# Optimization experiments

Hardware: AMD Instinct MI355X
Metric: run time of the kernel (lower is better)

## Reference

```python
import jax, jax.numpy as jnp
import numpy as np
from jax import lax

B = 256
NUM_CLASSES = 10
IN_CAPS = 32 * 6 * 6  # 1152
IN_DIM = 8
OUT_DIM = 16
NUM_ITERS = 3


def squash(t, axis=-1):
    sq = jnp.sum(t * t, axis=axis, keepdims=True)
    return (sq / (1.0 + sq)) * t / jnp.sqrt(sq)


def conv2d(x, w, b, stride):
    y = lax.conv_general_dilated(x, w, (stride, stride), 'VALID',
                                 dimension_numbers=('NCHW', 'OIHW', 'NCHW'))
    return y + b[None, :, None, None]


def setup_inputs() -> dict:
    key = jax.random.key(0)
    ks = jax.random.split(key, 12)
    f = jnp.float32
    return {
        'x': jax.random.uniform(ks[0], (B, 1, 28, 28), dtype=f),
        'conv1_w': jax.random.normal(ks[1], (256, 1, 9, 9), dtype=f) * 0.05,
        'conv1_b': jnp.zeros((256,), dtype=f),
        'prim_w': jax.random.normal(ks[2], (IN_DIM * 32, 256, 9, 9), dtype=f) * 0.02,
        'prim_b': jnp.zeros((IN_DIM * 32,), dtype=f),
        'route_w': jax.random.normal(ks[3], (NUM_CLASSES, IN_CAPS, IN_DIM, OUT_DIM), dtype=f),
        'dec_w1': jax.random.normal(ks[4], (OUT_DIM * NUM_CLASSES, 512), dtype=f) * 0.05,
        'dec_b1': jnp.zeros((512,), dtype=f),
        'dec_w2': jax.random.normal(ks[5], (512, 1024), dtype=f) * 0.04,
        'dec_b2': jnp.zeros((1024,), dtype=f),
        'dec_w3': jax.random.normal(ks[6], (1024, 28 * 28), dtype=f) * 0.03,
        'dec_b3': jnp.zeros((28 * 28,), dtype=f),
    }


def reference(x, conv1_w, conv1_b, prim_w, prim_b, route_w,
              dec_w1, dec_b1, dec_w2, dec_b2, dec_w3, dec_b3):
    bsz = x.shape[0]
    # conv1 + relu -> [B,256,20,20]
    h = jax.nn.relu(conv2d(x, conv1_w, conv1_b, 1))
    # primary capsules: 8 parallel convs (stacked into one) -> [B, 8*32, 6, 6]
    p = conv2d(h, prim_w, prim_b, 2)
    # each capsule conv flattens to [B, 32*36], concatenated along last dim
    p = p.reshape(bsz, IN_DIM, 32 * 6 * 6).transpose(0, 2, 1)  # [B, 1152, 8]
    u = squash(p, axis=-1)
    # priors: [o, b, i, d_out]
    priors = jnp.einsum('bic,oicd->obid', u, route_w)
    # routing by agreement: softmax over in_capsules (dim i), per original code
    logits = jnp.zeros((NUM_CLASSES, bsz, IN_CAPS, 1), dtype=priors.dtype)
    outputs = None
    for it in range(NUM_ITERS):
        probs = jax.nn.softmax(logits, axis=2)              # [o,b,i,1]
        outputs = squash(jnp.sum(probs * priors, axis=2, keepdims=True))  # [o,b,1,d]
        if it != NUM_ITERS - 1:
            logits = logits + jnp.sum(priors * outputs, axis=-1, keepdims=True)
    vecs = outputs.reshape(NUM_CLASSES, bsz, OUT_DIM).transpose(1, 0, 2)  # [B,10,16]
    classes = jnp.sqrt(jnp.sum(vecs * vecs, axis=-1))
    classes = jax.nn.softmax(classes, axis=1)               # [B,10]
    # y=None path: one-hot of predicted class (non-differentiable mask)
    y = jax.nn.one_hot(jnp.argmax(classes, axis=1), NUM_CLASSES, dtype=vecs.dtype)
    dec_in = (vecs * y[:, :, None]).reshape(bsz, -1)        # [B,160]
    hdec = jax.nn.relu(dec_in @ dec_w1 + dec_b1)
    hdec = jax.nn.relu(hdec @ dec_w2 + dec_b2)
    reconstruction = jax.nn.sigmoid(hdec @ dec_w3 + dec_b3)  # [B,784]
    return classes, reconstruction
```

## Files before the change

### kernel.cpp

```cpp
#include <hip/hip_runtime.h>
#include <hip/hip_bf16.h>
#include <math.h>


typedef __attribute__((ext_vector_type(8))) short bf16x8;
typedef __attribute__((ext_vector_type(4))) float f32x4;

__device__ __forceinline__ void gl16(const void* g, void* l) {
  __builtin_amdgcn_global_load_lds((const __attribute__((address_space(1))) void*)g,
                                   (__attribute__((address_space(3))) void*)l,
                                   16, 0, 0);
}

__global__ __launch_bounds__(256) void k_conv1(const float* __restrict__ x,
                                               const float* __restrict__ w,
                                               const float* __restrict__ bias,
                                               __hip_bfloat16* __restrict__ hT) {
  const int bid = blockIdx.x;
  const int img = bid >> 2, ocq = bid & 3;
  __shared__ float xs[784];
  __shared__ float ws[64 * 81];
  const int t = threadIdx.x;
  const float4* xg = (const float4*)(x + (size_t)img * 784);
  if (t < 196) ((float4*)xs)[t] = xg[t];
  const float4* wg = (const float4*)(w + (size_t)ocq * 64 * 81);
  for (int i = t; i < 1296; i += 256) ((float4*)ws)[i] = wg[i];
  __syncthreads();
  const int ocl = t & 63, rowg = t >> 6;
  const int oc = ocq * 64 + ocl;
  const int ch = oc >> 3, icl = oc & 7;
  const float bv = bias[oc];
  __hip_bfloat16* hb = hT + ((size_t)img * 32 + ch) * 6560 + icl;
#pragma unroll 1
  for (int r = rowg; r < 20; r += 4) {
    float acc[20];
#pragma unroll
    for (int p = 0; p < 20; p++) acc[p] = bv;
#pragma unroll
    for (int ky = 0; ky < 9; ky++) {
      float xr[28];
      const float* xrow = &xs[(r + ky) * 28];
#pragma unroll
      for (int q = 0; q < 7; q++) ((float4*)xr)[q] = ((const float4*)xrow)[q];
      float wr[9];
#pragma unroll
      for (int i = 0; i < 9; i++) wr[i] = ws[ocl * 81 + ky * 9 + i];
#pragma unroll
      for (int kx = 0; kx < 9; kx++)
#pragma unroll
        for (int p = 0; p < 20; p++)
          acc[p] = fmaf(wr[kx], xr[p + kx], acc[p]);
    }
#pragma unroll
    for (int p = 0; p < 20; p++) {
      const float v = fmaxf(acc[p], 0.f);
      const __hip_bfloat16 hi = __float2bfloat16(v);
      const __hip_bfloat16 lo = __float2bfloat16(v - __bfloat162float(hi));
      __hip_bfloat16* dst = hb + (size_t)(p * 41 + r * 2) * 8;
      dst[0] = hi;
      dst[8] = lo;
    }
  }
}

__global__ __launch_bounds__(256) void k_wrep(const float* __restrict__ pw,
                                              __hip_bfloat16* __restrict__ wGp) {
  const int s = blockIdx.x >> 2, ocq = blockIdx.x & 3;
  const int ch = s / 21, tq = s - ch * 21;
  __hip_bfloat16* outp = wGp + ((size_t)s * 4 + ocq) * 4608;
  const int t = threadIdx.x;
  for (int e = t; e < 2048; e += 256) {
    const int ocl = e >> 5, k = e & 31;
    const int tapl = k >> 3, icl = k & 7;
    const int tap = tq * 4 + tapl, ic = ch * 8 + icl;
    const int oc = ocq * 64 + ocl;
    const float v = (tap < 81) ? pw[((size_t)oc * 256 + ic) * 81 + tap] : 0.f;
    const __hip_bfloat16 hi = __float2bfloat16(v);
    const __hip_bfloat16 lo = __float2bfloat16(v - __bfloat162float(hi));
    outp[ocl * 72 + k] = hi;
    outp[ocl * 72 + 32 + k] = lo;
  }
  for (int e = t; e < 512; e += 256) {
    const int ocl = e >> 3, j = e & 7;
    outp[ocl * 72 + 64 + j] = __float2bfloat16(0.f);
  }
}

#define HT_B 52480
#define PQ_F 2359296
__global__ __launch_bounds__(512) void k_conv2(
    const __hip_bfloat16* __restrict__ hTg,
    const __hip_bfloat16* __restrict__ wGp,
    float* __restrict__ pq, int c0) {
  __shared__ char hT[HT_B];
  const int bid = blockIdx.x;
  int ig, ocq, kq;
  if (gridDim.x == 512) {
    ig = (bid & 7) | (((bid >> 5) & 7) << 3);
    ocq = (bid >> 3) & 3;
    kq = bid >> 8;
  } else {
    ig = bid >> 3;
    ocq = (bid >> 1) & 3;
    kq = bid & 1;
  }
  const int t = threadIdx.x;
  const int w = t >> 6, lane = t & 63;
  const int lquad = lane >> 4, lrow = lane & 15;
  const int mhalf = w >> 2;
  const int nt = mhalf ? 4 : 5;
  const int mtb = mhalf ? 5 : 0;
  const int ocg = ocq * 64 + (w & 3) * 16 + lrow;
  int abase[5];
#pragma unroll
  for (int i = 0; i < 5; i++) {
    int m = (mtb + i) * 16 + lrow;
    if (i >= nt) m = 0;
    const int img = m / 36, px = m - img * 36;
    const int oy = px / 6, ox = px - oy * 6;
    abase[i] = img * 13120 + ox * 1312 + oy * 64;
  }
  f32x4 acc[5];
#pragma unroll
  for (int i = 0; i < 5; i++) acc[i] = (f32x4){0.f, 0.f, 0.f, 0.f};

  const char* hgc = (const char*)hTg;
  const char* wp = (const char*)wGp + ((size_t)(kq * 336) * 4 + ocq) * 4608 +
                   ((w & 3) * 16 + lrow) * 144 + lquad * 16;
  bf16x8 bh = *(const bf16x8*)wp;
  bf16x8 bl = *(const bf16x8*)(wp + 64);
  wp += 18432;
#pragma unroll 1
  for (int chl = 0; chl < 16; chl++) {
    const int ch = kq * 16 + chl;
    const char* hch = hgc + ((size_t)(ig * 128) + ch) * 13120;
#pragma unroll
    for (int rr = 0; rr < 6; rr++) {
      const int idx = t + rr * 512;
      const int j = idx / 820, r = idx - j * 820;
      gl16(hch + (size_t)j * 419840 + r * 16, hT + rr * 8192 + w * 1024);
    }
    if (t < 208) {
      const int idx = 3072 + t;
      const int j = idx / 820, r = idx - j * 820;
      gl16(hch + (size_t)j * 419840 + r * 16, hT + 49152 + w * 1024);
    }
    __syncthreads();
#pragma unroll 1
    for (int tq = 0; tq < 21; tq++) {
      const bf16x8 nh = *(const bf16x8*)wp;
      const bf16x8 nl = *(const bf16x8*)(wp + 64);
      wp += 18432;
      const int tt = tq * 4 + lquad;
      const int ky = tt / 9, kx = tt - ky * 9;
      const int toff = kx * 656 + ky * 32;
      bf16x8 ah[5];
#pragma unroll
      for (int i = 0; i < 5; i++)
        ah[i] = *(const bf16x8*)(hT + abase[i] + toff);
#pragma unroll
      for (int i = 0; i < 5; i++)
        if (i < nt) acc[i] = __builtin_amdgcn_mfma_f32_16x16x32_bf16(ah[i], bh, acc[i], 0, 0, 0);
#pragma unroll
      for (int i = 0; i < 5; i++)
        if (i < nt) acc[i] = __builtin_amdgcn_mfma_f32_16x16x32_bf16(ah[i], bl, acc[i], 0, 0, 0);
      bf16x8 al[5];
#pragma unroll
      for (int i = 0; i < 5; i++)
        al[i] = *(const bf16x8*)(hT + abase[i] + toff + 16);
#pragma unroll
      for (int i = 0; i < 5; i++)
        if (i < nt) acc[i] = __builtin_amdgcn_mfma_f32_16x16x32_bf16(al[i], bh, acc[i], 0, 0, 0);
      bh = nh;
      bl = nl;
    }
    __syncthreads();
  }
  float* pblk = pq + (size_t)kq * PQ_F;
#pragma unroll
  for (int i = 0; i < 5; i++) {
    if (i < nt) {
#pragma unroll
      for (int r = 0; r < 4; r++) {
        const int m = (mtb + i) * 16 + lquad * 4 + r;
        const int img = m / 36, px = m - img * 36;
        pblk[((size_t)(c0 + ig * 4 + img) * 36 + px) * 256 + ocg] = acc[i][r];
      }
    }
  }
}

__global__ __launch_bounds__(256) void k_squash(const float* __restrict__ pq,
                                                const float* __restrict__ bias,
                                                float* __restrict__ u) {
  const int gid = blockIdx.x * 256 + threadIdx.x;
  const int b = gid / 1152, i = gid - b * 1152;
  const int cp = i / 36, px = i - cp * 36;
  const float* pb = pq + ((size_t)b * 36 + px) * 256 + cp;
  float s[8];
#pragma unroll
  for (int d = 0; d < 8; d++)
    s[d] = pb[d * 32] + pb[(size_t)PQ_F + d * 32] + bias[cp + d * 32];
  float sq = 0.f;
#pragma unroll
  for (int d = 0; d < 8; d++) sq = fmaf(s[d], s[d], sq);
  const float scale = sq / ((1.f + sq) * sqrtf(sq));
  float o[8];
#pragma unroll
  for (int d = 0; d < 8; d++) o[d] = s[d] * scale;
  float* ub = u + (size_t)gid * 8;
  ((float4*)ub)[0] = ((float4*)o)[0];
  ((float4*)ub)[1] = ((float4*)o)[1];
}

__device__ __forceinline__ float wsum(float v) {
#pragma unroll
  for (int o = 32; o > 0; o >>= 1) v += __shfl_xor(v, o, 64);
  return v;
}
__device__ __forceinline__ float wmaxr(float v) {
#pragma unroll
  for (int o = 32; o > 0; o >>= 1) v = fmaxf(v, __shfl_xor(v, o, 64));
  return v;
}

__global__ __launch_bounds__(256) void k_route(const float* __restrict__ u,
                                               const float* __restrict__ rw,
                                               float* __restrict__ vecs) {
  const int o = blockIdx.x >> 8, b = blockIdx.x & 255;
  __shared__ float us[9216];
  __shared__ float red[4 * 17];
  __shared__ float redm[4];
  const int t = threadIdx.x;
  const int wave = t >> 6, lane = t & 63;
  {
    const float4* ub = (const float4*)(u + (size_t)b * 9216);
    for (int i = t; i < 2304; i += 256) ((float4*)us)[i] = ub[i];
  }
  __syncthreads();
  float pri[5][16];
  const float* rwo = rw + (size_t)o * 147456;
#pragma unroll
  for (int ci = 0; ci < 5; ci++) {
    const bool valid = (ci < 4) || (t < 128);
    const int i = valid ? (t + ci * 256) : 0;
    const float* rwi = rwo + (size_t)i * 128;
    float a[16];
#pragma unroll
    for (int d = 0; d < 16; d++) a[d] = 0.f;
#pragma unroll
    for (int c = 0; c < 8; c++) {
      const float uv = us[i * 8 + c];
      const float4* r4 = (const float4*)(rwi + c * 16);
      const float4 p0 = r4[0], p1 = r4[1], p2 = r4[2], p3 = r4[3];
      a[0] = fmaf(uv, p0.x, a[0]);  a[1] = fmaf(uv, p0.y, a[1]);
      a[2] = fmaf(uv, p0.z, a[2]);  a[3] = fmaf(uv, p0.w, a[3]);
      a[4] = fmaf(uv, p1.x, a[4]);  a[5] = fmaf(uv, p1.y, a[5]);
      a[6] = fmaf(uv, p1.z, a[6]);  a[7] = fmaf(uv, p1.w, a[7]);
      a[8] = fmaf(uv, p2.x, a[8]);  a[9] = fmaf(uv, p2.y, a[9]);
      a[10] = fmaf(uv, p2.z, a[10]); a[11] = fmaf(uv, p2.w, a[11]);
      a[12] = fmaf(uv, p3.x, a[12]); a[13] = fmaf(uv, p3.y, a[13]);
      a[14] = fmaf(uv, p3.z, a[14]); a[15] = fmaf(uv, p3.w, a[15]);
    }
#pragma unroll
    for (int d = 0; d < 16; d++) pri[ci][d] = valid ? a[d] : 0.f;
  }
  float l[5];
#pragma unroll
  for (int ci = 0; ci < 5; ci++)
    l[ci] = ((ci < 4) || (t < 128)) ? 0.f : -1e30f;
  float v[16];
#pragma unroll 1
  for (int it = 0; it < 3; it++) {
    float m = l[0];
#pragma unroll
    for (int ci = 1; ci < 5; ci++) m = fmaxf(m, l[ci]);
    m = wmaxr(m);
    if (lane == 0) redm[wave] = m;
    __syncthreads();
    m = fmaxf(fmaxf(redm[0], redm[1]), fmaxf(redm[2], redm[3]));
    float Z = 0.f, S[16];
#pragma unroll
    for (int d = 0; d < 16; d++) S[d] = 0.f;
#pragma unroll
    for (int ci = 0; ci < 5; ci++) {
      const float e = expf(l[ci] - m);
      Z += e;
#pragma unroll
      for (int d = 0; d < 16; d++) S[d] = fmaf(e, pri[ci][d], S[d]);
    }
    Z = wsum(Z);
#pragma unroll
    for (int d = 0; d < 16; d++) S[d] = wsum(S[d]);
    __syncthreads();
    if (lane == 0) {
      red[wave * 17] = Z;
#pragma unroll
      for (int d = 0; d < 16; d++) red[wave * 17 + 1 + d] = S[d];
    }
    __syncthreads();
    const float Zt = red[0] + red[17] + red[34] + red[51];
    float sv[16], sq = 0.f;
#pragma unroll
    for (int d = 0; d < 16; d++) {
      const float sd = (red[1 + d] + red[18 + d] + red[35 + d] + red[52 + d]) / Zt;
      sv[d] = sd;
      sq = fmaf(sd, sd, sq);
    }
    const float scale = sq / ((1.f + sq) * sqrtf(sq));
#pragma unroll
    for (int d = 0; d < 16; d++) v[d] = scale * sv[d];
    if (it < 2) {
#pragma unroll
      for (int ci = 0; ci < 5; ci++) {
        float dot = 0.f;
#pragma unroll
        for (int d = 0; d < 16; d++) dot = fmaf(pri[ci][d], v[d], dot);
        l[ci] += dot;
      }
    }
  }
  if (t == 0) {
    float* vb = vecs + ((size_t)b * 10 + o) * 16;
#pragma unroll
    for (int d = 0; d < 16; d++) vb[d] = v[d];
  }
}

__global__ __launch_bounds__(64) void k_cls(const float* __restrict__ vecs,
                                            float* __restrict__ out,
                                            float* __restrict__ selvec,
                                            int* __restrict__ amv) {
  const int b = blockIdx.x * 64 + threadIdx.x;
  const float* vb = vecs + (size_t)b * 160;
  float n[10];
#pragma unroll
  for (int o = 0; o < 10; o++) {
    float sq = 0.f;
#pragma unroll
    for (int d = 0; d < 16; d++) { const float xv = vb[o * 16 + d]; sq = fmaf(xv, xv, sq); }
    n[o] = sqrtf(sq);
  }
  float m = n[0];
#pragma unroll
  for (int o = 1; o < 10; o++) m = fmaxf(m, n[o]);
  float e[10], Z = 0.f;
#pragma unroll
  for (int o = 0; o < 10; o++) { e[o] = expf(n[o] - m); Z += e[o]; }
  const float inv = 1.f / Z;
  float cls[10];
#pragma unroll
  for (int o = 0; o < 10; o++) {
    cls[o] = e[o] * inv;
    out[(size_t)b * 10 + o] = cls[o];
  }
  int am = 0;
  float best = cls[0];
#pragma unroll
  for (int o = 1; o < 10; o++)
    if (cls[o] > best) { best = cls[o]; am = o; }
  amv[b] = am;
#pragma unroll
  for (int d = 0; d < 16; d++) selvec[(size_t)b * 16 + d] = vb[am * 16 + d];
}

__global__ __launch_bounds__(512) void k_dec1(const float* __restrict__ selvec,
                                              const int* __restrict__ amv,
                                              const float* __restrict__ w1,
                                              const float* __restrict__ b1,
                                              float* __restrict__ h1) {
  const int b = blockIdx.x, t = threadIdx.x;
  __shared__ float sv[16];
  __shared__ int ams;
  if (t < 16) sv[t] = selvec[(size_t)b * 16 + t];
  if (t == 0) ams = amv[b];
  __syncthreads();
  const float* wrow = w1 + (size_t)ams * 16 * 512;
  float acc = b1[t];
#pragma unroll
  for (int d = 0; d < 16; d++) acc = fmaf(sv[d], wrow[d * 512 + t], acc);
  h1[(size_t)b * 512 + t] = fmaxf(acc, 0.f);
}

__global__ __launch_bounds__(128) void k_dec2(const float* __restrict__ h1,
                                              const float* __restrict__ w2,
                                              const float* __restrict__ b2,
                                              float* __restrict__ h2) {
  const int nc = blockIdx.x >> 5, bg = blockIdx.x & 31;
  const int t = threadIdx.x;
  const int n = nc * 128 + t;
  const int bs = bg * 8;
  __shared__ float h1s[8 * 512];
  __shared__ float wts[32 * 128];
  {
    const float4* src = (const float4*)(h1 + (size_t)bs * 512);
    for (int i = t; i < 1024; i += 128) ((float4*)h1s)[i] = src[i];
  }
  float acc[8];
  const float bb = b2[n];
#pragma unroll
  for (int j = 0; j < 8; j++) acc[j] = bb;
#pragma unroll 1
  for (int kt = 0; kt < 16; kt++) {
    __syncthreads();
#pragma unroll
    for (int r = 0; r < 32; r++)
      wts[r * 128 + t] = w2[(size_t)(kt * 32 + r) * 1024 + n];
    __syncthreads();
#pragma unroll
    for (int k4 = 0; k4 < 8; k4++) {
      float wq[4];
#pragma unroll
      for (int q = 0; q < 4; q++) wq[q] = wts[(k4 * 4 + q) * 128 + t];
#pragma unroll
      for (int j = 0; j < 8; j++) {
        const float4 hv = *(const float4*)&h1s[j * 512 + kt * 32 + k4 * 4];
        acc[j] = fmaf(hv.x, wq[0], acc[j]);
        acc[j] = fmaf(hv.y, wq[1], acc[j]);
        acc[j] = fmaf(hv.z, wq[2], acc[j]);
        acc[j] = fmaf(hv.w, wq[3], acc[j]);
      }
    }
  }
#pragma unroll
  for (int j = 0; j < 8; j++) h2[(size_t)(bs + j) * 1024 + n] = fmaxf(acc[j], 0.f);
}

__global__ __launch_bounds__(128) void k_dec3(const float* __restrict__ h2,
                                              const float* __restrict__ w3,
                                              const float* __restrict__ b3,
                                              float* __restrict__ out) {
  const int nc = blockIdx.x >> 5, bg = blockIdx.x & 31;
  const int t = threadIdx.x;
  const int bs = bg * 8;
  __shared__ float h2s[8 * 1024];
  __shared__ float wts[32 * 112];
  {
    const float4* src = (const float4*)(h2 + (size_t)bs * 1024);
    for (int i = t; i < 2048; i += 128) ((float4*)h2s)[i] = src[i];
  }
  const int n = nc * 112 + (t < 112 ? t : 0);
  float acc[8];
  const float bb = b3[n];
#pragma unroll
  for (int j = 0; j < 8; j++) acc[j] = bb;
#pragma unroll 1
  for (int kt = 0; kt < 32; kt++) {
    __syncthreads();
#pragma unroll
    for (int r = 0; r < 32; r++)
      if (t < 112) wts[r * 112 + t] = w3[(size_t)(kt * 32 + r) * 784 + n];
    __syncthreads();
    if (t < 112) {
#pragma unroll
      for (int k4 = 0; k4 < 8; k4++) {
        float wq[4];
#pragma unroll
        for (int q = 0; q < 4; q++) wq[q] = wts[(k4 * 4 + q) * 112 + t];
#pragma unroll
        for (int j = 0; j < 8; j++) {
          const float4 hv = *(const float4*)&h2s[j * 1024 + kt * 32 + k4 * 4];
          acc[j] = fmaf(hv.x, wq[0], acc[j]);
          acc[j] = fmaf(hv.y, wq[1], acc[j]);
          acc[j] = fmaf(hv.z, wq[2], acc[j]);
          acc[j] = fmaf(hv.w, wq[3], acc[j]);
        }
      }
    }
  }
  if (t < 112) {
#pragma unroll
    for (int j = 0; j < 8; j++)
      out[(size_t)(bs + j) * 784 + n] = 1.f / (1.f + expf(-acc[j]));
  }
}

extern "C" void kernel_launch(void* const* d_in, const int* in_sizes, int n_in,
                              void* d_out, int out_size, void* d_ws, size_t ws_size,
                              hipStream_t stream) {
  const float* x   = (const float*)d_in[0];
  const float* c1w = (const float*)d_in[1];
  const float* c1b = (const float*)d_in[2];
  const float* pw  = (const float*)d_in[3];
  const float* pb  = (const float*)d_in[4];
  const float* rw  = (const float*)d_in[5];
  const float* w1  = (const float*)d_in[6];
  const float* b1  = (const float*)d_in[7];
  const float* w2  = (const float*)d_in[8];
  const float* b2  = (const float*)d_in[9];
  const float* w3  = (const float*)d_in[10];
  const float* b3  = (const float*)d_in[11];
  float* out = (float*)d_out;
  float* ws = (float*)d_ws;

  const size_t WGP_F = ((size_t)672 * 4 * 4608 + 18432) / 4;
  const size_t U_F = 2359296;
  const size_t SMALL_F = 40960 + 4096 + 256 + 131072 + 262144;
  const size_t fixed_f = WGP_F + 2 * PQ_F + U_F + SMALL_F;
  int chunk = 256;
  while (chunk > 8 && (fixed_f + (size_t)chunk * 104960) * 4 > ws_size) chunk >>= 1;

  __hip_bfloat16* wGp  = (__hip_bfloat16*)ws;
  __hip_bfloat16* hTgc = (__hip_bfloat16*)(ws + WGP_F);
  float* pq   = ws + WGP_F + (size_t)chunk * 104960;
  float* u    = pq + 2 * PQ_F;
  float* vecs = u + U_F;
  float* sel  = vecs + 40960;
  int*   amv  = (int*)(sel + 4096);
  float* h1   = sel + 4096 + 256;
  float* h2   = h1 + 131072;

  k_wrep<<<dim3(2688), dim3(256), 0, stream>>>(pw, wGp);
  for (int c0 = 0; c0 < 256; c0 += chunk) {
    k_conv1<<<dim3(chunk * 4), dim3(256), 0, stream>>>(x + (size_t)c0 * 784, c1w, c1b, hTgc);
    k_conv2<<<dim3((chunk / 4) * 8), dim3(512), 0, stream>>>(hTgc, wGp, pq, c0);
  }
  k_squash<<<dim3(1152), dim3(256), 0, stream>>>(pq, pb, u);
  k_route<<<dim3(2560), dim3(256), 0, stream>>>(u, rw, vecs);
  k_cls<<<dim3(4), dim3(64), 0, stream>>>(vecs, out, sel, amv);
  k_dec1<<<dim3(256), dim3(512), 0, stream>>>(sel, amv, w1, b1, h1);
  k_dec2<<<dim3(256), dim3(128), 0, stream>>>(h1, w2, b2, h2);
  k_dec3<<<dim3(224), dim3(128), 0, stream>>>(h2, w3, b3, out + 2560);
}
```

Baseline: 867.8 us.

## Stage conv1 output through LDS for coalesced stores; transpose routing weights

conv1 now writes its bf16 hi/lo results into a shared-memory tile and then emits them to global memory as 16-byte vector stores, replacing scattered 2-byte stores. A new k_rrep kernel transposes route_w to a [o][c*d][i] layout so that k_route threads, each handling a different input capsule, read consecutive addresses. This removes strided per-thread weight loads. The cost is an extra transpose kernel launch, extra workspace, and two block barriers per row iteration in conv1.

```diff
diff --git a/kernel.cpp b/kernel.cpp
--- a/kernel.cpp
+++ b/kernel.cpp
@@ -20,6 +20,7 @@
   const int img = bid >> 2, ocq = bid & 3;
   __shared__ float xs[784];
   __shared__ float ws[64 * 81];
+  __shared__ __attribute__((aligned(16))) __hip_bfloat16 tile[8 * 1288];
   const int t = threadIdx.x;
   const float4* xg = (const float4*)(x + (size_t)img * 784);
   if (t < 196) ((float4*)xs)[t] = xg[t];
@@ -28,11 +29,12 @@
   __syncthreads();
   const int ocl = t & 63, rowg = t >> 6;
   const int oc = ocq * 64 + ocl;
-  const int ch = oc >> 3, icl = oc & 7;
+  const int chl = ocl >> 3, icl = ocl & 7;
   const float bv = bias[oc];
-  __hip_bfloat16* hb = hT + ((size_t)img * 32 + ch) * 6560 + icl;
+  __hip_bfloat16* hb = hT + ((size_t)img * 32 + ocq * 8) * 6560;
 #pragma unroll 1
-  for (int r = rowg; r < 20; r += 4) {
+  for (int it = 0; it < 5; it++) {
+    const int r = it * 4 + rowg;
     float acc[20];
 #pragma unroll
     for (int p = 0; p < 20; p++) acc[p] = bv;
@@ -56,10 +58,19 @@
       const float v = fmaxf(acc[p], 0.f);
       const __hip_bfloat16 hi = __float2bfloat16(v);
       const __hip_bfloat16 lo = __float2bfloat16(v - __bfloat162float(hi));
-      __hip_bfloat16* dst = hb + (size_t)(p * 41 + r * 2) * 8;
-      dst[0] = hi;
-      dst[8] = lo;
-    }
+      tile[chl * 1288 + (p * 8 + rowg * 2) * 8 + icl] = hi;
+      tile[chl * 1288 + (p * 8 + rowg * 2 + 1) * 8 + icl] = lo;
+    }
+    __syncthreads();
+#pragma unroll
+    for (int q = 0; q < 5; q++) {
+      const int idx = q * 256 + t;
+      const int c2 = idx / 160, rem = idx - c2 * 160;
+      const int xx = rem >> 3, j = rem & 7;
+      const float4 vdat = *(const float4*)&tile[c2 * 1288 + rem * 8];
+      *(float4*)(hb + (size_t)c2 * 6560 + (size_t)(xx * 41 + it * 8 + j) * 8) = vdat;
+    }
+    __syncthreads();
   }
 }
 
@@ -83,6 +94,22 @@
   for (int e = t; e < 512; e += 256) {
     const int ocl = e >> 3, j = e & 7;
     outp[ocl * 72 + 64 + j] = __float2bfloat16(0.f);
+  }
+}
+
+__global__ __launch_bounds__(256) void k_rrep(const float* __restrict__ rw,
+                                              float* __restrict__ rwT) {
+  const int o = blockIdx.x / 18, ig = blockIdx.x % 18;
+  __shared__ float tile[64 * 129];
+  const int t = threadIdx.x;
+  for (int idx = t; idx < 64 * 128; idx += 256) {
+    const int i = idx >> 7, cd = idx & 127;
+    tile[i * 129 + cd] = rw[((size_t)o * 1152 + ig * 64 + i) * 128 + cd];
+  }
+  __syncthreads();
+  for (int idx = t; idx < 64 * 128; idx += 256) {
+    const int cd = idx >> 6, il = idx & 63;
+    rwT[((size_t)o * 128 + cd) * 1152 + ig * 64 + il] = tile[il * 129 + cd];
   }
 }
 
@@ -225,7 +252,7 @@
 }
 
 __global__ __launch_bounds__(256) void k_route(const float* __restrict__ u,
-                                               const float* __restrict__ rw,
+                                               const float* __restrict__ rwT,
                                                float* __restrict__ vecs) {
   const int o = blockIdx.x >> 8, b = blockIdx.x & 255;
   __shared__ float us[9216];
@@ -239,28 +266,21 @@
   }
   __syncthreads();
   float pri[5][16];
-  const float* rwo = rw + (size_t)o * 147456;
+  const float* rwo = rwT + (size_t)o * 128 * 1152;
 #pragma unroll
   for (int ci = 0; ci < 5; ci++) {
     const bool valid = (ci < 4) || (t < 128);
     const int i = valid ? (t + ci * 256) : 0;
-    const float* rwi = rwo + (size_t)i * 128;
     float a[16];
 #pragma unroll
     for (int d = 0; d < 16; d++) a[d] = 0.f;
 #pragma unroll
     for (int c = 0; c < 8; c++) {
       const float uv = us[i * 8 + c];
-      const float4* r4 = (const float4*)(rwi + c * 16);
-      const float4 p0 = r4[0], p1 = r4[1], p2 = r4[2], p3 = r4[3];
-      a[0] = fmaf(uv, p0.x, a[0]);  a[1] = fmaf(uv, p0.y, a[1]);
-      a[2] = fmaf(uv, p0.z, a[2]);  a[3] = fmaf(uv, p0.w, a[3]);
-      a[4] = fmaf(uv, p1.x, a[4]);  a[5] = fmaf(uv, p1.y, a[5]);
-      a[6] = fmaf(uv, p1.z, a[6]);  a[7] = fmaf(uv, p1.w, a[7]);
-      a[8] = fmaf(uv, p2.x, a[8]);  a[9] = fmaf(uv, p2.y, a[9]);
-      a[10] = fmaf(uv, p2.z, a[10]); a[11] = fmaf(uv, p2.w, a[11]);
-      a[12] = fmaf(uv, p3.x, a[12]); a[13] = fmaf(uv, p3.y, a[13]);
-      a[14] = fmaf(uv, p3.z, a[14]); a[15] = fmaf(uv, p3.w, a[15]);
+      const float* wcol = rwo + (size_t)(c * 16) * 1152 + i;
+#pragma unroll
+      for (int d = 0; d < 16; d++)
+        a[d] = fmaf(uv, wcol[(size_t)d * 1152], a[d]);
     }
 #pragma unroll
     for (int d = 0; d < 16; d++) pri[ci][d] = valid ? a[d] : 0.f;
@@ -495,8 +515,9 @@
 
   const size_t WGP_F = ((size_t)672 * 4 * 4608 + 18432) / 4;
   const size_t U_F = 2359296;
+  const size_t RWT_F = 10 * 128 * 1152;
   const size_t SMALL_F = 40960 + 4096 + 256 + 131072 + 262144;
-  const size_t fixed_f = WGP_F + 2 * PQ_F + U_F + SMALL_F;
+  const size_t fixed_f = WGP_F + 2 * PQ_F + U_F + RWT_F + SMALL_F;
   int chunk = 256;
   while (chunk > 8 && (fixed_f + (size_t)chunk * 104960) * 4 > ws_size) chunk >>= 1;
 
@@ -504,19 +525,21 @@
   __hip_bfloat16* hTgc = (__hip_bfloat16*)(ws + WGP_F);
   float* pq   = ws + WGP_F + (size_t)chunk * 104960;
   float* u    = pq + 2 * PQ_F;
-  float* vecs = u + U_F;
+  float* rwT  = u + U_F;
+  float* vecs = rwT + RWT_F;
   float* sel  = vecs + 40960;
   int*   amv  = (int*)(sel + 4096);
   float* h1   = sel + 4096 + 256;
   float* h2   = h1 + 131072;
 
   k_wrep<<<dim3(2688), dim3(256), 0, stream>>>(pw, wGp);
+  k_rrep<<<dim3(180), dim3(256), 0, stream>>>(rw, rwT);
   for (int c0 = 0; c0 < 256; c0 += chunk) {
     k_conv1<<<dim3(chunk * 4), dim3(256), 0, stream>>>(x + (size_t)c0 * 784, c1w, c1b, hTgc);
     k_conv2<<<dim3((chunk / 4) * 8), dim3(512), 0, stream>>>(hTgc, wGp, pq, c0);
   }
   k_squash<<<dim3(1152), dim3(256), 0, stream>>>(pq, pb, u);
-  k_route<<<dim3(2560), dim3(256), 0, stream>>>(u, rw, vecs);
+  k_route<<<dim3(2560), dim3(256), 0, stream>>>(u, rwT, vecs);
   k_cls<<<dim3(4), dim3(64), 0, stream>>>(vecs, out, sel, amv);
   k_dec1<<<dim3(256), dim3(512), 0, stream>>>(sel, amv, w1, b1, h1);
   k_dec2<<<dim3(256), dim3(128), 0, stream>>>(h1, w2, b2, h2);
```

Result: slower. 960.0 us (+10.6%).
